# Optimization experiments

Measured on AMD Instinct MI355X. Metric: run time of the kernel, lower is better.

Reference implementation:

```python
import jax, jax.numpy as jnp
import numpy as np

HID = 128          # hidden_dim
NF = 8             # n_features of reconstructed PathFeatureExtractor
S0 = 100.0
T = 1.0
XI0 = 0.235 ** 2
ETA_REF = 1.9
DELTA_IDX = 3      # PathFeatureExtractor.DELTA_PREV_INDEX
NEG_SLOPE = 0.2


def _features(S):
    """Causal per-step path features. S: (B, n+1) -> (B, n, NF)."""
    B, np1 = S.shape
    n = np1 - 1
    logm = jnp.log(S / S0)                       # (B, n+1) log-moneyness
    x = logm[:, :n]                              # value at step k
    ret = jnp.diff(logm, axis=1)                 # (B, n) log returns
    qv_full = jnp.cumsum(ret ** 2, axis=1)
    qv = jnp.concatenate([jnp.zeros((B, 1), S.dtype), qv_full[:, :-1]], axis=1)  # QV up to step k
    k = jnp.arange(n, dtype=S.dtype)
    t = k / n * T
    tau = (T - t) / T                            # normalized time to maturity
    run_mean = jnp.cumsum(x, axis=1) / (k + 1.0)
    ones = jnp.ones_like(x)
    feats = jnp.stack([
        x,                                       # 0: log(S_k/S0)
        tau * ones,                              # 1: time to maturity
        jnp.sqrt(XI0) * ones,                    # 2: ref vol
        jnp.zeros_like(x),                       # 3: delta_prev slot (injected in scan)
        run_mean,                                # 4: running mean log-price (sig level 1)
        qv,                                      # 5: realized quadratic variation (sig level 2 diag)
        ETA_REF * jnp.sqrt(qv + 1e-12),          # 6: vol-of-vol scaled QV
        (t / T) * ones,                          # 7: elapsed time
    ], axis=-1)
    return feats


def _mlp(feat, W0, b0, rW1, rb1, rW2, rb2, sW1, sb1, sW2, sb2, Wf, bf):
    lrelu = lambda v: jax.nn.leaky_relu(v, NEG_SLOPE)
    h = lrelu(feat @ W0 + b0)
    h = h + (lrelu(h @ rW1 + rb1) @ rW2 + rb2)   # ResidualBlock 1
    h = h + (lrelu(h @ sW1 + sb1) @ sW2 + sb2)   # ResidualBlock 2
    return jax.nn.sigmoid(h @ Wf + bf)[:, 0]


def _linear_params(key, fan_in, fan_out):
    kw, kb = jax.random.split(key)
    bound = 1.0 / np.sqrt(fan_in)
    W = jax.random.uniform(kw, (fan_in, fan_out), jnp.float32, -bound, bound)
    b = jax.random.uniform(kb, (fan_out,), jnp.float32, -bound, bound)
    return W, b


def setup_inputs() -> dict:
    key = jax.random.key(0)
    ks = jax.random.split(key, 6)
    B, n = 32768, 64
    # GBM-like price paths starting at S0
    incr = 0.02 * jax.random.normal(ks[0], (B, n), jnp.float32)
    logpath = jnp.concatenate([jnp.zeros((B, 1), jnp.float32), jnp.cumsum(incr, axis=1)], axis=1)
    S = S0 * jnp.exp(logpath)
    W0, b0 = _linear_params(ks[1], NF, HID)
    rW1, rb1 = _linear_params(ks[2], HID, HID)
    rW2, rb2 = _linear_params(jax.random.fold_in(ks[2], 1), HID, HID)
    sW1, sb1 = _linear_params(ks[3], HID, HID)
    sW2, sb2 = _linear_params(jax.random.fold_in(ks[3], 1), HID, HID)
    Wf, bf = _linear_params(ks[4], HID, 1)
    return {"S": S, "W0": W0, "b0": b0, "rW1": rW1, "rb1": rb1, "rW2": rW2, "rb2": rb2,
            "sW1": sW1, "sb1": sb1, "sW2": sW2, "sb2": sb2, "Wf": Wf, "bf": bf}


def reference(S, W0, b0, rW1, rb1, rW2, rb2, sW1, sb1, sW2, sb2, Wf, bf):
    feats = _features(S).astype(jnp.float32)          # (B, n, NF)
    fT = jnp.transpose(feats, (1, 0, 2))              # (n, B, NF) for scan
    B = S.shape[0]

    def step(delta_prev, feat_k):
        # inject detached delta_{k-1} at feature index 3 (matches .detach())
        feat_k = feat_k.at[:, DELTA_IDX].set(jax.lax.stop_gradient(delta_prev))
        d = _mlp(feat_k, W0, b0, rW1, rb1, rW2, rb2, sW1, sb1, sW2, sb2, Wf, bf)
        return d, d

    _, deltas = jax.lax.scan(step, jnp.zeros((B,), jnp.float32), fT)
    return jnp.transpose(deltas)                      # (B, n)
```

## Files before the change

kernel.cpp:

```cpp
#include <hip/hip_runtime.h>
#include <math.h>

#define HID 128
#define NSTEPS 64
#define SLEN 65
#define THREADS 256
#define ROWS 64
#define ASTRIDE 136
#define FSTRIDE 40
#define DSTR 68

typedef _Float16 half8 __attribute__((ext_vector_type(8)));
typedef __fp16 fp16x2 __attribute__((ext_vector_type(2)));
typedef float floatx4 __attribute__((ext_vector_type(4)));

__global__ __launch_bounds__(THREADS, 2)
void hedger(const float* __restrict__ S,
            const float* __restrict__ W0,  const float* __restrict__ b0,
            const float* __restrict__ rW1, const float* __restrict__ rb1,
            const float* __restrict__ rW2, const float* __restrict__ rb2,
            const float* __restrict__ sW1, const float* __restrict__ sb1,
            const float* __restrict__ sW2, const float* __restrict__ sb2,
            const float* __restrict__ Wf,  const float* __restrict__ bfp,
            float* __restrict__ out)
{
  __shared__ __align__(16) _Float16 bufA[ROWS * ASTRIDE];
  __shared__ __align__(16) _Float16 bufB[ROWS * ASTRIDE];
  __shared__ __align__(16) _Float16 bufC[ROWS * ASTRIDE];
  __shared__ __align__(16) _Float16 featb[ROWS * FSTRIDE];
  __shared__ __align__(16) _Float16 WfS[HID];
  __shared__ __align__(16) _Float16 WfuS[HID];
  __shared__ __align__(16) _Float16 Ws2S[HID];
  __shared__             float    CvalS;
  __shared__ __align__(16) float    deltab[ROWS * DSTR];

  const int tid  = threadIdx.x;
  const int wave = tid >> 6;
  const int lane = tid & 63;
  const int l15  = lane & 15;
  const int quad = lane >> 4;
  const int n_base = wave * 32;
  const int r0 = blockIdx.x * ROWS;
  const int col0 = n_base + 2 * l15;

  half8 wfrag[3][4][2];
  {
    const float* Wm[2] = {rW1, sW1};
#pragma unroll
    for (int m = 0; m < 2; ++m)
#pragma unroll
      for (int kq = 0; kq < 4; ++kq)
#pragma unroll
        for (int nt = 0; nt < 2; ++nt) {
          const int n  = col0 + nt;
          const int kb = kq * 32 + quad * 8;
          half8 f;
#pragma unroll
          for (int j = 0; j < 8; ++j)
            f[j] = (_Float16)Wm[m][(kb + j) * HID + n];
          wfrag[m][kq][nt] = f;
        }
  }
  half8 w0frag[2];
#pragma unroll
  for (int nt = 0; nt < 2; ++nt) {
    const int n = col0 + nt;
    half8 f;
#pragma unroll
    for (int j = 0; j < 8; ++j) {
      const int k = quad * 8 + j;
      f[j] = (k < 8) ? (_Float16)W0[k * HID + n] : (_Float16)0.f;
    }
    w0frag[nt] = f;
  }
  float b0r[2], rb1r[2], cv[2];
#pragma unroll
  for (int nt = 0; nt < 2; ++nt) {
    const int n = col0 + nt;
    b0r[nt] = b0[n]; rb1r[nt] = rb1[n];
    float p = 0.f;
#pragma unroll
    for (int kq = 0; kq < 4; ++kq) {
      const int kb = kq * 32 + quad * 8;
#pragma unroll
      for (int j = 0; j < 8; ++j)
        p += rb2[kb + j] * (float)wfrag[1][kq][nt][j];
    }
    p += __shfl_xor(p, 16);
    p += __shfl_xor(p, 32);
    cv[nt] = p + sb1[n];
  }

  for (int i = tid; i < ROWS * FSTRIDE; i += THREADS) featb[i] = (_Float16)0.f;
  if (tid < HID) {
    WfS[tid] = (_Float16)Wf[tid];
    float su = 0.f, ss = 0.f;
    for (int n = 0; n < HID; ++n) {
      su += rW2[tid * HID + n] * Wf[n];
      ss += sW2[tid * HID + n] * Wf[n];
    }
    WfuS[tid] = (_Float16)su;
    Ws2S[tid] = (_Float16)ss;
  }
  if (wave == 0) {
    float p = (rb2[lane] + sb2[lane]) * Wf[lane]
            + (rb2[lane + 64] + sb2[lane + 64]) * Wf[lane + 64];
    p += __shfl_xor(p, 1);  p += __shfl_xor(p, 2);  p += __shfl_xor(p, 4);
    p += __shfl_xor(p, 8);  p += __shfl_xor(p, 16); p += __shfl_xor(p, 32);
    if (lane == 0) CvalS = p + bfp[0];
  }

  floatx4 acc[4][2];

#define INIT_BIAS(BR) do { \
  _Pragma("unroll") for (int mt = 0; mt < 4; ++mt) \
  _Pragma("unroll") for (int nt = 0; nt < 2; ++nt) { \
    floatx4 z = {BR[nt], BR[nt], BR[nt], BR[nt]}; acc[mt][nt] = z; } } while (0)

#define GEMM128(SRC, MI) do { \
  _Pragma("unroll") for (int kq = 0; kq < 4; ++kq) { \
    half8 afr[4]; \
    _Pragma("unroll") for (int mt = 0; mt < 4; ++mt) \
      afr[mt] = *(const half8*)&SRC[(mt * 16 + l15) * ASTRIDE + kq * 32 + quad * 8]; \
    _Pragma("unroll") for (int mt = 0; mt < 4; ++mt) \
    _Pragma("unroll") for (int nt = 0; nt < 2; ++nt) \
      acc[mt][nt] = __builtin_amdgcn_mfma_f32_16x16x32_f16( \
          afr[mt], wfrag[MI][kq][nt], acc[mt][nt], 0, 0, 0); \
  } } while (0)

#define EPI_LRELU(DST) do { \
  _Pragma("unroll") for (int mt = 0; mt < 4; ++mt) \
  _Pragma("unroll") for (int r = 0; r < 4; ++r) { \
    const int row = mt * 16 + quad * 4 + r; \
    const float v0 = acc[mt][0][r]; \
    const float v1 = acc[mt][1][r]; \
    fp16x2 h2 = {(__fp16)fmaxf(v0, 0.2f * v0), (__fp16)fmaxf(v1, 0.2f * v1)}; \
    *(fp16x2*)&DST[row * ASTRIDE + col0] = h2; \
  } } while (0)

#define EPI_STORE(DST) do { \
  _Pragma("unroll") for (int mt = 0; mt < 4; ++mt) \
  _Pragma("unroll") for (int r = 0; r < 4; ++r) { \
    const int row = mt * 16 + quad * 4 + r; \
    fp16x2 h2 = {(__fp16)acc[mt][0][r], (__fp16)acc[mt][1][r]}; \
    *(fp16x2*)&DST[row * ASTRIDE + col0] = h2; \
  } } while (0)

#pragma unroll
  for (int h = 0; h < 2; ++h) {
    __syncthreads();
    for (int i = tid; i < ROWS * HID; i += THREADS) {
      const int row = i >> 7, c = i & 127;
      bufA[row * ASTRIDE + c] = (_Float16)rW2[(h * 64 + row) * HID + c];
    }
    __syncthreads();
    {
      float zr[2] = {0.f, 0.f};
      INIT_BIAS(zr);
      GEMM128(bufA, 1);
      EPI_STORE(bufB);
    }
    __syncthreads();
#pragma unroll
    for (int kqh = 0; kqh < 2; ++kqh) {
      const int kq = h * 2 + kqh;
      half8 f0, f1;
#pragma unroll
      for (int j = 0; j < 8; ++j) {
        const int kl = kq * 32 + quad * 8 + j - h * 64;
        const fp16x2 p = *(const fp16x2*)&bufB[kl * ASTRIDE + col0];
        f0[j] = (_Float16)p[0];
        f1[j] = (_Float16)p[1];
      }
      wfrag[2][kq][0] = f0;
      wfrag[2][kq][1] = f1;
    }
  }
  __syncthreads();

  float lm_prev = 0.f, cum_x = 0.f, qv = 0.f;
  const float* Srow = S + (size_t)(r0 + (tid & (ROWS - 1))) * SLEN;
  if (tid < ROWS) {
    const float lm = logf(Srow[0] * 0.01f);
    lm_prev = lm; cum_x = lm; qv = 0.f;
    _Float16* fr = &featb[tid * FSTRIDE];
    fr[0] = (_Float16)lm;
    fr[1] = (_Float16)1.0f;
    fr[2] = (_Float16)0.235f;
    fr[3] = (_Float16)0.f;
    fr[4] = (_Float16)lm;
    fr[5] = (_Float16)0.f;
    fr[6] = (_Float16)(1.9f * sqrtf(1e-12f));
    fr[7] = (_Float16)0.f;
  }
  __syncthreads();
  const float Cval = CvalS;

#pragma unroll 1
  for (int k = 0; k < NSTEPS; ++k) {
    INIT_BIAS(b0r);
    {
      half8 afr[4];
#pragma unroll
      for (int mt = 0; mt < 4; ++mt)
        afr[mt] = *(const half8*)&featb[(mt * 16 + l15) * FSTRIDE + quad * 8];
#pragma unroll
      for (int mt = 0; mt < 4; ++mt)
#pragma unroll
        for (int nt = 0; nt < 2; ++nt)
          acc[mt][nt] = __builtin_amdgcn_mfma_f32_16x16x32_f16(
              afr[mt], w0frag[nt], acc[mt][nt], 0, 0, 0);
    }
    EPI_LRELU(bufA);
    __syncthreads();

    if (tid < ROWS) {
      const int kk = k + 1;
      const float lm = logf(Srow[kk] * 0.01f);
      const float rr = lm - lm_prev; qv += rr * rr;
      lm_prev = lm; cum_x += lm;
      const float tT = (float)kk * (1.f / 64.f);
      _Float16* fr = &featb[tid * FSTRIDE];
      fr[0] = (_Float16)lm;
      fr[1] = (_Float16)(1.f - tT);
      fr[4] = (_Float16)(cum_x / (float)(kk + 1));
      fr[5] = (_Float16)qv;
      fr[6] = (_Float16)(1.9f * sqrtf(qv + 1e-12f));
      fr[7] = (_Float16)tT;
    }

    INIT_BIAS(rb1r);  GEMM128(bufA, 0);  EPI_LRELU(bufB);
    __syncthreads();

    INIT_BIAS(cv);
    GEMM128(bufA, 1);
    GEMM128(bufB, 2);
    EPI_LRELU(bufC);
    __syncthreads();

    {
      floatx4 d1 = {0.f, 0.f, 0.f, 0.f};
      floatx4 d2 = {0.f, 0.f, 0.f, 0.f};
      floatx4 d3 = {0.f, 0.f, 0.f, 0.f};
      const int arow = (wave * 16 + l15) * ASTRIDE;
#pragma unroll
      for (int kq = 0; kq < 4; ++kq) {
        const int off = kq * 32 + quad * 8;
        const half8 a1 = *(const half8*)&bufA[arow + off];
        const half8 w1 = *(const half8*)&WfS[off];
        d1 = __builtin_amdgcn_mfma_f32_16x16x32_f16(a1, w1, d1, 0, 0, 0);
        const half8 a2 = *(const half8*)&bufB[arow + off];
        const half8 w2 = *(const half8*)&WfuS[off];
        d2 = __builtin_amdgcn_mfma_f32_16x16x32_f16(a2, w2, d2, 0, 0, 0);
        const half8 a3 = *(const half8*)&bufC[arow + off];
        const half8 w3 = *(const half8*)&Ws2S[off];
        d3 = __builtin_amdgcn_mfma_f32_16x16x32_f16(a3, w3, d3, 0, 0, 0);
      }
      if (l15 < 4) {
        const float s1 = (l15 & 2) ? ((l15 & 1) ? d1[3] : d1[2])
                                   : ((l15 & 1) ? d1[1] : d1[0]);
        const float s2 = (l15 & 2) ? ((l15 & 1) ? d2[3] : d2[2])
                                   : ((l15 & 1) ? d2[1] : d2[0]);
        const float s3 = (l15 & 2) ? ((l15 & 1) ? d3[3] : d3[2])
                                   : ((l15 & 1) ? d3[1] : d3[0]);
        const int row = wave * 16 + quad * 4 + l15;
        const float d = 1.f / (1.f + expf(-(s1 + s2 + s3 + Cval)));
        featb[row * FSTRIDE + 3] = (_Float16)d;
        deltab[row * DSTR + k] = d;
      }
    }
    __syncthreads();
  }

  {
    const int row = tid >> 2;
    const int c0  = (tid & 3) * 16;
    const float* dr = &deltab[row * DSTR + c0];
    float* orow = &out[(size_t)(r0 + row) * NSTEPS + c0];
#pragma unroll
    for (int u = 0; u < 4; ++u) {
      const floatx4 v = *(const floatx4*)&dr[u * 4];
      *(floatx4*)&orow[u * 4] = v;
    }
  }
#undef INIT_BIAS
#undef GEMM128
#undef EPI_LRELU
#undef EPI_STORE
}

extern "C" void kernel_launch(void* const* d_in, const int* in_sizes, int n_in,
                              void* d_out, int out_size, void* d_ws, size_t ws_size,
                              hipStream_t stream) {
  const float* S   = (const float*)d_in[0];
  const float* W0  = (const float*)d_in[1];
  const float* b0  = (const float*)d_in[2];
  const float* rW1 = (const float*)d_in[3];
  const float* rb1 = (const float*)d_in[4];
  const float* rW2 = (const float*)d_in[5];
  const float* rb2 = (const float*)d_in[6];
  const float* sW1 = (const float*)d_in[7];
  const float* sb1 = (const float*)d_in[8];
  const float* sW2 = (const float*)d_in[9];
  const float* sb2 = (const float*)d_in[10];
  const float* Wf  = (const float*)d_in[11];
  const float* bf  = (const float*)d_in[12];
  float* out = (float*)d_out;

  const int B = out_size / NSTEPS;
  const int nblocks = B / ROWS;
  hedger<<<nblocks, THREADS, 0, stream>>>(
      S, W0, b0, rW1, rb1, rW2, rb2, sW1, sb1, sW2, sb2, Wf, bf, out);
}
```

Measured before the change: 340.8 us.

## Halve rows per block to 32 and raise occupancy to four blocks per CU

Cuts the batch rows handled per workgroup from 64 to 32, which doubles the grid size and raises the launch-bounds occupancy hint from 2 to 4 blocks per CU. The per-wave MFMA tiling drops from 4 to 2 row tiles, the accumulators become named scalars, the weight-fold precompute loop is rebuilt in four 32-row passes, and the output head runs only on the first two waves. The aim is to expose more parallel blocks for the serial 64-step recurrence and to lower register and LDS use per block. The trade-off is that each block now repeats the same weight load and fold setup for half as many rows.

```diff
diff --git a/kernel.cpp b/kernel.cpp
--- a/kernel.cpp
+++ b/kernel.cpp
@@ -5,7 +5,7 @@
 #define NSTEPS 64
 #define SLEN 65
 #define THREADS 256
-#define ROWS 64
+#define ROWS 32
 #define ASTRIDE 136
 #define FSTRIDE 40
 #define DSTR 68
@@ -14,7 +14,7 @@
 typedef __fp16 fp16x2 __attribute__((ext_vector_type(2)));
 typedef float floatx4 __attribute__((ext_vector_type(4)));
 
-__global__ __launch_bounds__(THREADS, 2)
+__global__ __launch_bounds__(THREADS, 4)
 void hedger(const float* __restrict__ S,
             const float* __restrict__ W0,  const float* __restrict__ b0,
             const float* __restrict__ rW1, const float* __restrict__ rb1,
@@ -110,48 +110,50 @@
     if (lane == 0) CvalS = p + bfp[0];
   }
 
-  floatx4 acc[4][2];
+  floatx4 acc[2];
+
+  floatx4 acc00, acc01, acc10, acc11;
+#define ACC(MT, NT) acc##MT##NT
 
 #define INIT_BIAS(BR) do { \
-  _Pragma("unroll") for (int mt = 0; mt < 4; ++mt) \
-  _Pragma("unroll") for (int nt = 0; nt < 2; ++nt) { \
-    floatx4 z = {BR[nt], BR[nt], BR[nt], BR[nt]}; acc[mt][nt] = z; } } while (0)
+  floatx4 z0 = {BR[0], BR[0], BR[0], BR[0]}; \
+  floatx4 z1 = {BR[1], BR[1], BR[1], BR[1]}; \
+  ACC(0,0) = z0; ACC(0,1) = z1; ACC(1,0) = z0; ACC(1,1) = z1; } while (0)
 
 #define GEMM128(SRC, MI) do { \
   _Pragma("unroll") for (int kq = 0; kq < 4; ++kq) { \
-    half8 afr[4]; \
-    _Pragma("unroll") for (int mt = 0; mt < 4; ++mt) \
-      afr[mt] = *(const half8*)&SRC[(mt * 16 + l15) * ASTRIDE + kq * 32 + quad * 8]; \
-    _Pragma("unroll") for (int mt = 0; mt < 4; ++mt) \
-    _Pragma("unroll") for (int nt = 0; nt < 2; ++nt) \
-      acc[mt][nt] = __builtin_amdgcn_mfma_f32_16x16x32_f16( \
-          afr[mt], wfrag[MI][kq][nt], acc[mt][nt], 0, 0, 0); \
+    const half8 af0 = *(const half8*)&SRC[(l15) * ASTRIDE + kq * 32 + quad * 8]; \
+    const half8 af1 = *(const half8*)&SRC[(16 + l15) * ASTRIDE + kq * 32 + quad * 8]; \
+    ACC(0,0) = __builtin_amdgcn_mfma_f32_16x16x32_f16(af0, wfrag[MI][kq][0], ACC(0,0), 0, 0, 0); \
+    ACC(0,1) = __builtin_amdgcn_mfma_f32_16x16x32_f16(af0, wfrag[MI][kq][1], ACC(0,1), 0, 0, 0); \
+    ACC(1,0) = __builtin_amdgcn_mfma_f32_16x16x32_f16(af1, wfrag[MI][kq][0], ACC(1,0), 0, 0, 0); \
+    ACC(1,1) = __builtin_amdgcn_mfma_f32_16x16x32_f16(af1, wfrag[MI][kq][1], ACC(1,1), 0, 0, 0); \
   } } while (0)
 
-#define EPI_LRELU(DST) do { \
-  _Pragma("unroll") for (int mt = 0; mt < 4; ++mt) \
+#define EPI_LRELU_MT(DST, MT) do { \
   _Pragma("unroll") for (int r = 0; r < 4; ++r) { \
-    const int row = mt * 16 + quad * 4 + r; \
-    const float v0 = acc[mt][0][r]; \
-    const float v1 = acc[mt][1][r]; \
+    const int row = MT * 16 + quad * 4 + r; \
+    const float v0 = ACC(MT,0)[r]; \
+    const float v1 = ACC(MT,1)[r]; \
     fp16x2 h2 = {(__fp16)fmaxf(v0, 0.2f * v0), (__fp16)fmaxf(v1, 0.2f * v1)}; \
     *(fp16x2*)&DST[row * ASTRIDE + col0] = h2; \
   } } while (0)
-
-#define EPI_STORE(DST) do { \
-  _Pragma("unroll") for (int mt = 0; mt < 4; ++mt) \
+#define EPI_LRELU(DST) do { EPI_LRELU_MT(DST, 0); EPI_LRELU_MT(DST, 1); } while (0)
+
+#define EPI_STORE_MT(DST, MT) do { \
   _Pragma("unroll") for (int r = 0; r < 4; ++r) { \
-    const int row = mt * 16 + quad * 4 + r; \
-    fp16x2 h2 = {(__fp16)acc[mt][0][r], (__fp16)acc[mt][1][r]}; \
+    const int row = MT * 16 + quad * 4 + r; \
+    fp16x2 h2 = {(__fp16)ACC(MT,0)[r], (__fp16)ACC(MT,1)[r]}; \
     *(fp16x2*)&DST[row * ASTRIDE + col0] = h2; \
   } } while (0)
-
-#pragma unroll
-  for (int h = 0; h < 2; ++h) {
+#define EPI_STORE(DST) do { EPI_STORE_MT(DST, 0); EPI_STORE_MT(DST, 1); } while (0)
+
+#pragma unroll
+  for (int p = 0; p < 4; ++p) {
     __syncthreads();
     for (int i = tid; i < ROWS * HID; i += THREADS) {
       const int row = i >> 7, c = i & 127;
-      bufA[row * ASTRIDE + c] = (_Float16)rW2[(h * 64 + row) * HID + c];
+      bufA[row * ASTRIDE + c] = (_Float16)rW2[(p * 32 + row) * HID + c];
     }
     __syncthreads();
     {
@@ -161,19 +163,17 @@
       EPI_STORE(bufB);
     }
     __syncthreads();
-#pragma unroll
-    for (int kqh = 0; kqh < 2; ++kqh) {
-      const int kq = h * 2 + kqh;
+    {
       half8 f0, f1;
 #pragma unroll
       for (int j = 0; j < 8; ++j) {
-        const int kl = kq * 32 + quad * 8 + j - h * 64;
-        const fp16x2 p = *(const fp16x2*)&bufB[kl * ASTRIDE + col0];
-        f0[j] = (_Float16)p[0];
-        f1[j] = (_Float16)p[1];
+        const int kl = quad * 8 + j;
+        const fp16x2 pr = *(const fp16x2*)&bufB[kl * ASTRIDE + col0];
+        f0[j] = (_Float16)pr[0];
+        f1[j] = (_Float16)pr[1];
       }
-      wfrag[2][kq][0] = f0;
-      wfrag[2][kq][1] = f1;
+      wfrag[2][p][0] = f0;
+      wfrag[2][p][1] = f1;
     }
   }
   __syncthreads();
@@ -200,16 +200,12 @@
   for (int k = 0; k < NSTEPS; ++k) {
     INIT_BIAS(b0r);
     {
-      half8 afr[4];
-#pragma unroll
-      for (int mt = 0; mt < 4; ++mt)
-        afr[mt] = *(const half8*)&featb[(mt * 16 + l15) * FSTRIDE + quad * 8];
-#pragma unroll
-      for (int mt = 0; mt < 4; ++mt)
-#pragma unroll
-        for (int nt = 0; nt < 2; ++nt)
-          acc[mt][nt] = __builtin_amdgcn_mfma_f32_16x16x32_f16(
-              afr[mt], w0frag[nt], acc[mt][nt], 0, 0, 0);
+      const half8 af0 = *(const half8*)&featb[(l15) * FSTRIDE + quad * 8];
+      const half8 af1 = *(const half8*)&featb[(16 + l15) * FSTRIDE + quad * 8];
+      ACC(0,0) = __builtin_amdgcn_mfma_f32_16x16x32_f16(af0, w0frag[0], ACC(0,0), 0, 0, 0);
+      ACC(0,1) = __builtin_amdgcn_mfma_f32_16x16x32_f16(af0, w0frag[1], ACC(0,1), 0, 0, 0);
+      ACC(1,0) = __builtin_amdgcn_mfma_f32_16x16x32_f16(af1, w0frag[0], ACC(1,0), 0, 0, 0);
+      ACC(1,1) = __builtin_amdgcn_mfma_f32_16x16x32_f16(af1, w0frag[1], ACC(1,1), 0, 0, 0);
     }
     EPI_LRELU(bufA);
     __syncthreads();
@@ -238,7 +234,7 @@
     EPI_LRELU(bufC);
     __syncthreads();
 
-    {
+    if (wave < 2) {
       floatx4 d1 = {0.f, 0.f, 0.f, 0.f};
       floatx4 d2 = {0.f, 0.f, 0.f, 0.f};
       floatx4 d3 = {0.f, 0.f, 0.f, 0.f};
@@ -273,12 +269,12 @@
   }
 
   {
-    const int row = tid >> 2;
-    const int c0  = (tid & 3) * 16;
+    const int row = tid >> 3;
+    const int c0  = (tid & 7) * 8;
     const float* dr = &deltab[row * DSTR + c0];
     float* orow = &out[(size_t)(r0 + row) * NSTEPS + c0];
 #pragma unroll
-    for (int u = 0; u < 4; ++u) {
+    for (int u = 0; u < 2; ++u) {
       const floatx4 v = *(const floatx4*)&dr[u * 4];
       *(floatx4*)&orow[u * 4] = v;
     }
@@ -286,7 +282,10 @@
 #undef INIT_BIAS
 #undef GEMM128
 #undef EPI_LRELU
+#undef EPI_LRELU_MT
 #undef EPI_STORE
+#undef EPI_STORE_MT
+#undef ACC
 }
 
 extern "C" void kernel_launch(void* const* d_in, const int* in_sizes, int n_in,
```

Result: slower. 672.8 us (+97.4%).
